# Kernel tuning notes

Measured on AMD Instinct MI355X. Metric: run time of the kernel, lower is better.

## Reference

```python
import jax, jax.numpy as jnp
import numpy as np

D_MODEL = 1024
HEADS = 16
D_HEAD = D_MODEL // HEADS


def relative_shift(score):
    # score: [b, h, n, 2n-1] -> [b, h, n, n] via the pad/reshape skew trick
    b, h, n, r = score.shape  # r == 2n - 1
    score = jnp.pad(score, ((0, 0), (0, 0), (0, 0), (1, 0)))  # [b,h,n,2n]
    score = score.reshape(b, h, n * 2 * n)[:, :, n:].reshape(b, h, n, 2 * n - 1)
    return score[..., :n]


def setup_inputs() -> dict:
    key = jax.random.key(0)
    ks = jax.random.split(key, 16)
    b, n, d = 4, 1024, D_MODEL
    s = 1.0 / np.sqrt(d)
    inp = {
        "query": jax.random.normal(ks[0], (b, n, d), jnp.float32),
        "key": jax.random.normal(ks[1], (b, n, d), jnp.float32),
        "value": jax.random.normal(ks[2], (b, n, d), jnp.float32),
        "pos_emb": jax.random.normal(ks[3], (b, 2 * n - 1, d), jnp.float32),
        "Wq": jax.random.normal(ks[4], (d, d), jnp.float32) * s,
        "bq": jnp.zeros((d,), jnp.float32),
        "Wk": jax.random.normal(ks[5], (d, d), jnp.float32) * s,
        "bk": jnp.zeros((d,), jnp.float32),
        "Wv": jax.random.normal(ks[6], (d, d), jnp.float32) * s,
        "bv": jnp.zeros((d,), jnp.float32),
        "Wo": jax.random.normal(ks[7], (d, d), jnp.float32) * s,
        "bo": jnp.zeros((d,), jnp.float32),
        "Wp": jax.random.normal(ks[8], (d, d), jnp.float32) * s,  # pos_proj, no bias
        "u_bias": jax.random.normal(ks[9], (HEADS, D_HEAD), jnp.float32) * 0.05,
        "v_bias": jax.random.normal(ks[10], (HEADS, D_HEAD), jnp.float32) * 0.05,
    }
    return inp


def reference(query, key, value, pos_emb, Wq, bq, Wk, bk, Wv, bv, Wo, bo, Wp, u_bias, v_bias):
    b, n, d = query.shape
    h, dh = HEADS, D_HEAD
    q = (query @ Wq + bq).reshape(b, n, h, dh)            # [b,n,h,dh]
    k = (key @ Wk + bk).reshape(b, n, h, dh)              # [b,n,h,dh]
    v = (value @ Wv + bv).reshape(b, n, h, dh)            # [b,n,h,dh]
    p = (pos_emb @ Wp).reshape(b, 2 * n - 1, h, dh)       # [b,2n-1,h,dh]

    content_score = jnp.einsum('bnhd,bmhd->bhnm', q + u_bias, k)   # [b,h,n,n]
    pos_score = jnp.einsum('bnhd,brhd->bhnr', q + v_bias, p)        # [b,h,n,2n-1]
    pos_score = relative_shift(pos_score)                           # [b,h,n,n]

    score = (content_score + pos_score) / jnp.sqrt(jnp.asarray(d, score_dtype := query.dtype))
    attn = jax.nn.softmax(score, axis=-1)                 # dropout p=0.0 -> identity
    out = jnp.einsum('bhnm,bmhd->bnhd', attn, v).reshape(b, n, d)
    out = out @ Wo + bo
    return out, attn, content_score, pos_score
```

## Files before the change

kernel.cpp:

```cpp
#include <hip/hip_runtime.h>
#include <hip/hip_bf16.h>

typedef __bf16 bf16;
typedef __attribute__((ext_vector_type(8))) __bf16 bf16x8;
typedef __attribute__((ext_vector_type(4))) float f32x4;

#define DEV static __device__ __forceinline__

namespace {

constexpr int B = 4, N = 1024, D = 1024, H = 16, DH = 64;
constexpr int R2 = 2 * N - 1;
constexpr int BH = B * H;
constexpr float SCL = 0.03125f;

DEV bf16 f2b(float x) {
  unsigned u = __builtin_bit_cast(unsigned, x);
  unsigned r = u + 0x7FFFu + ((u >> 16) & 1u);
  unsigned short h = (unsigned short)(r >> 16);
  return __builtin_bit_cast(bf16, h);
}

DEV unsigned cvtpk(float lo, float hi) {
  unsigned r;
  asm("v_cvt_pk_bf16_f32 %0, %1, %2" : "=v"(r) : "v"(lo), "v"(hi));
  return r;
}

DEV bf16x8 cvt8pk(float4 a, float4 b) {
  union { unsigned u[4]; bf16x8 v; } r;
  r.u[0] = cvtpk(a.x, a.y); r.u[1] = cvtpk(a.z, a.w);
  r.u[2] = cvtpk(b.x, b.y); r.u[3] = cvtpk(b.z, b.w);
  return r.v;
}

DEV f32x4 mfma16(bf16x8 a, bf16x8 b, f32x4 c) {
  return __builtin_amdgcn_mfma_f32_16x16x32_bf16(a, b, c, 0, 0, 0);
}

DEV void nt_store4(float4 v, float* p) {
  f32x4 x = {v.x, v.y, v.z, v.w};
  __builtin_nontemporal_store(x, reinterpret_cast<f32x4*>(p));
}

DEV void block_sync_lds() {
  __builtin_amdgcn_sched_barrier(0);
  asm volatile("s_waitcnt lgkmcnt(0)" ::: "memory");
  __builtin_amdgcn_s_barrier();
  __builtin_amdgcn_sched_barrier(0);
}

__global__ __launch_bounds__(256) void transpose_cast_w(
    const float* __restrict__ w0, const float* __restrict__ w1,
    const float* __restrict__ w2, const float* __restrict__ w3,
    const float* __restrict__ w4, bf16* __restrict__ t0, bf16* __restrict__ t1,
    bf16* __restrict__ t2, bf16* __restrict__ t3, bf16* __restrict__ t4) {
  const float* src; bf16* dst;
  switch (blockIdx.z) {
    case 0: src = w0; dst = t0; break;
    case 1: src = w1; dst = t1; break;
    case 2: src = w2; dst = t2; break;
    case 3: src = w3; dst = t3; break;
    default: src = w4; dst = t4; break;
  }
  __shared__ float tile[64][65];
  const int k0 = blockIdx.y * 64, n0 = blockIdx.x * 64;
  const int t = threadIdx.x, r = t >> 2, c0 = (t & 3) * 16;
  const float4* sp = reinterpret_cast<const float4*>(src + (size_t)(k0 + r) * D + n0 + c0);
#pragma unroll
  for (int q = 0; q < 4; ++q) {
    float4 v = sp[q];
    tile[r][c0 + q * 4 + 0] = v.x; tile[r][c0 + q * 4 + 1] = v.y;
    tile[r][c0 + q * 4 + 2] = v.z; tile[r][c0 + q * 4 + 3] = v.w;
  }
  __syncthreads();
  union { unsigned u[8]; uint4 q[2]; } pk;
#pragma unroll
  for (int e = 0; e < 8; ++e)
    pk.u[e] = cvtpk(tile[c0 + 2 * e][r], tile[c0 + 2 * e + 1][r]);
  uint4* dp = reinterpret_cast<uint4*>(dst + (size_t)(n0 + r) * D + k0 + c0);
  dp[0] = pk.q[0]; dp[1] = pk.q[1];
}

enum { M_QUV = 0, M_HEAD = 1, M_P = 2, M_OUT = 3, M_V = 4 };

template <bool ABF>
DEV void proj_core(char* smem, const void* __restrict__ Av,
                   const bf16* __restrict__ Bt, int M, int mt, int nt, int mode,
                   const float* __restrict__ bias, const float* __restrict__ ubp,
                   const float* __restrict__ vbp, bf16* __restrict__ dst0,
                   bf16* __restrict__ dst1, float* __restrict__ outf) {
  bf16* As = (bf16*)smem;
  bf16* Bs = (bf16*)(smem + 16384);
  float* ep = (float*)smem;
  const int t = threadIdx.x;
  const int m0 = mt * 128, n0 = nt * 128;
  const int lane = t & 63, w = t >> 6;
  const int wi = w >> 1, wj = w & 1;
  const int fr = lane & 15, g = lane >> 4;
  f32x4 acc[4][4] = {};

  int rowc[4], ccc[4], rmc[4];
#pragma unroll
  for (int it = 0; it < 4; ++it) {
    const int chunk = it * 256 + t;
    rowc[it] = chunk >> 3; ccc[it] = chunk & 7;
    int rm = m0 + rowc[it]; rmc[it] = rm < M ? rm : M - 1;
  }
  float4 raf[4][2];
  bf16x8 rab[4];
  bf16x8 rbb[4];
  auto loadstep = [&](int k0) {
#pragma unroll
    for (int it = 0; it < 4; ++it) {
      if (ABF) {
        rab[it] = *reinterpret_cast<const bf16x8*>(
            (const bf16*)Av + (size_t)rmc[it] * D + k0 + ccc[it] * 8);
      } else {
        const float4* ap = reinterpret_cast<const float4*>(
            (const float*)Av + (size_t)rmc[it] * D + k0 + ccc[it] * 8);
        raf[it][0] = ap[0]; raf[it][1] = ap[1];
      }
      rbb[it] = *reinterpret_cast<const bf16x8*>(
          Bt + (size_t)(n0 + rowc[it]) * D + k0 + ccc[it] * 8);
    }
  };

  loadstep(0);
  for (int k0 = 0; k0 < D; k0 += 64) {
#pragma unroll
    for (int it = 0; it < 4; ++it) {
      const int row = rowc[it], cc = ccc[it];
      bf16x8 av;
      if (ABF) av = rab[it]; else av = cvt8pk(raf[it][0], raf[it][1]);
      *reinterpret_cast<bf16x8*>(&As[row * 64 + ((cc ^ (row & 7)) << 3)]) = av;
      *reinterpret_cast<bf16x8*>(&Bs[row * 64 + ((cc ^ (row & 7)) << 3)]) =
          rbb[it];
    }
    block_sync_lds();
    if (k0 + 64 < D) loadstep(k0 + 64);
#pragma unroll
    for (int ks = 0; ks < 2; ++ks) {
      bf16x8 fa[4], fb[4];
#pragma unroll
      for (int i = 0; i < 4; ++i) {
        const int row = wi * 64 + i * 16 + fr;
        fa[i] = *reinterpret_cast<const bf16x8*>(
            &As[row * 64 + (((ks * 4 + g) ^ (row & 7)) << 3)]);
      }
#pragma unroll
      for (int j = 0; j < 4; ++j) {
        const int row = wj * 64 + j * 16 + fr;
        fb[j] = *reinterpret_cast<const bf16x8*>(
            &Bs[row * 64 + (((ks * 4 + g) ^ (row & 7)) << 3)]);
      }
#pragma unroll
      for (int i = 0; i < 4; ++i)
#pragma unroll
        for (int j = 0; j < 4; ++j) acc[i][j] = mfma16(fa[i], fb[j], acc[i][j]);
    }
    block_sync_lds();
  }
#pragma unroll
  for (int p = 0; p < 2; ++p) {
    block_sync_lds();
    if (wi == p) {
#pragma unroll
      for (int i = 0; i < 4; ++i)
#pragma unroll
        for (int j = 0; j < 4; ++j)
#pragma unroll
          for (int q = 0; q < 4; ++q)
            ep[(i * 16 + g * 4 + q) * 132 + wj * 64 + j * 16 + fr] =
                acc[i][j][q];
    }
    block_sync_lds();
    if (mode == M_V) {
      const int col = t >> 1, seg = t & 1;
      const int cg = n0 + col;
      const int h_ = cg >> 6, dh = cg & 63;
      const int b_ = m0 >> 10;
      const int tok0 = (m0 & 1023) + p * 64 + seg * 32;
      const float bvv = bias[cg];
      unsigned pk[16];
#pragma unroll
      for (int e = 0; e < 16; ++e) {
        const float v0 = ep[(seg * 32 + 2 * e + 0) * 132 + col] + bvv;
        const float v1 = ep[(seg * 32 + 2 * e + 1) * 132 + col] + bvv;
        pk[e] = cvtpk(v0, v1);
      }
      bf16* dp = dst0 + ((size_t)(b_ * H + h_) * DH + dh) * N + tok0;
#pragma unroll
      for (int kk = 0; kk < 4; ++kk)
        reinterpret_cast<uint4*>(dp)[kk] =
            *reinterpret_cast<const uint4*>(&pk[kk * 4]);
      continue;
    }
    const int lr = t >> 2, cl = (t & 3) * 32;
    const int m = m0 + p * 64 + lr;
    if (m < M) {
      float v[32];
#pragma unroll
      for (int kk = 0; kk < 8; ++kk) {
        const float4 f =
            *reinterpret_cast<const float4*>(&ep[lr * 132 + cl + kk * 4]);
        v[kk * 4 + 0] = f.x; v[kk * 4 + 1] = f.y;
        v[kk * 4 + 2] = f.z; v[kk * 4 + 3] = f.w;
      }
      const int cg0 = n0 + cl;
      if (mode == M_OUT) {
        float* op = outf + (size_t)m * D + cg0;
#pragma unroll
        for (int kk = 0; kk < 8; ++kk) {
          float4 f = {v[kk * 4] + bias[cg0 + kk * 4],
                      v[kk * 4 + 1] + bias[cg0 + kk * 4 + 1],
                      v[kk * 4 + 2] + bias[cg0 + kk * 4 + 2],
                      v[kk * 4 + 3] + bias[cg0 + kk * 4 + 3]};
          nt_store4(f, op + kk * 4);
        }
      } else if (mode == M_P) {
        const int b_ = m / R2, r_ = m - b_ * R2;
        const int h_ = cg0 >> 6, dh0 = cg0 & 63;
        bf16* dp = dst0 + (((size_t)(b_ * H + h_)) * R2 + r_) * DH + dh0;
        unsigned pk[16];
#pragma unroll
        for (int e = 0; e < 16; ++e) pk[e] = cvtpk(v[2 * e], v[2 * e + 1]);
#pragma unroll
        for (int kk = 0; kk < 4; ++kk)
          reinterpret_cast<uint4*>(dp)[kk] =
              *reinterpret_cast<const uint4*>(&pk[kk * 4]);
      } else {
        const int b_ = m >> 10, ii = m & (N - 1);
        const int h_ = cg0 >> 6, dh0 = cg0 & 63;
        const size_t o = (((size_t)(b_ * H + h_)) * N + ii) * DH + dh0;
        if (mode == M_QUV) {
          unsigned pku[16], pkv[16];
#pragma unroll
          for (int e = 0; e < 16; ++e) {
            const float b0 = bias[cg0 + 2 * e], b1 = bias[cg0 + 2 * e + 1];
            pku[e] = cvtpk(v[2 * e] + b0 + ubp[cg0 + 2 * e],
                           v[2 * e + 1] + b1 + ubp[cg0 + 2 * e + 1]);
            pkv[e] = cvtpk(v[2 * e] + b0 + vbp[cg0 + 2 * e],
                           v[2 * e + 1] + b1 + vbp[cg0 + 2 * e + 1]);
          }
#pragma unroll
          for (int kk = 0; kk < 4; ++kk) {
            reinterpret_cast<uint4*>(dst0 + o)[kk] =
                *reinterpret_cast<const uint4*>(&pku[kk * 4]);
            reinterpret_cast<uint4*>(dst1 + o)[kk] =
                *reinterpret_cast<const uint4*>(&pkv[kk * 4]);
          }
        } else {
          unsigned pk[16];
#pragma unroll
          for (int e = 0; e < 16; ++e)
            pk[e] = cvtpk(v[2 * e] + bias[cg0 + 2 * e],
                          v[2 * e + 1] + bias[cg0 + 2 * e + 1]);
#pragma unroll
          for (int kk = 0; kk < 4; ++kk)
            reinterpret_cast<uint4*>(dst0 + o)[kk] =
                *reinterpret_cast<const uint4*>(&pk[kk * 4]);
        }
      }
    }
  }
}

__global__ __launch_bounds__(256, 3) void proj_qkvp(
    const float* __restrict__ query, const float* __restrict__ key,
    const float* __restrict__ value, const float* __restrict__ pos_emb,
    const bf16* __restrict__ Wqt, const bf16* __restrict__ Wkt,
    const bf16* __restrict__ Wvt, const bf16* __restrict__ Wpt,
    const float* __restrict__ bq, const float* __restrict__ bk,
    const float* __restrict__ bv, const float* __restrict__ ub,
    const float* __restrict__ vbp, bf16* __restrict__ Qu,
    bf16* __restrict__ Qv, bf16* __restrict__ Kb, bf16* __restrict__ Vt,
    bf16* __restrict__ Pb) {
  __shared__ __align__(16) char smem[34048];
  const int z = blockIdx.z, x = blockIdx.x, y = blockIdx.y;
  const int nt = y & 7;
  const int mt = x * 4 + (y >> 3);
  switch (z) {
    case 0:
      proj_core<false>(smem, query, Wqt, B * N, mt, nt, M_QUV, bq, ub, vbp, Qu,
                       Qv, nullptr);
      break;
    case 1:
      proj_core<false>(smem, key, Wkt, B * N, mt, nt, M_HEAD, bk, nullptr,
                       nullptr, Kb, nullptr, nullptr);
      break;
    case 2:
      proj_core<false>(smem, value, Wvt, B * N, mt, nt, M_V, bv, nullptr,
                       nullptr, Vt, nullptr, nullptr);
      break;
    case 3:
      proj_core<false>(smem, pos_emb, Wpt, B * R2, mt, nt, M_P, nullptr,
                       nullptr, nullptr, Pb, nullptr, nullptr);
      break;
    default:
      proj_core<false>(smem, pos_emb, Wpt, B * R2, 32 + mt, nt, M_P, nullptr,
                       nullptr, nullptr, Pb, nullptr, nullptr);
      break;
  }
}

__global__ __launch_bounds__(256, 2) void proj_out(const bf16* __restrict__ OA,
                                                   const bf16* __restrict__ Wot,
                                                   const float* __restrict__ bo,
                                                   float* __restrict__ outF) {
  __shared__ __align__(16) char smem[34048];
  const int nt = blockIdx.y & 7;
  const int mt = blockIdx.x * 4 + (blockIdx.y >> 3);
  proj_core<true>(smem, OA, Wot, B * N, mt, nt, M_OUT, bo, nullptr, nullptr,
                  nullptr, nullptr, outF);
}

constexpr int RB = 16;

DEV int SIDX(int r, int c) {
  return r * 1024 + (((c >> 2) ^ (r & 7)) << 2) + (c & 3);
}

__global__ __launch_bounds__(512, 4) void fused_attn(
    const bf16* __restrict__ Qu, const bf16* __restrict__ Qv,
    const bf16* __restrict__ Kb, const bf16* __restrict__ Pb,
    const bf16* __restrict__ Vt, float* __restrict__ cont,
    float* __restrict__ posS, float* __restrict__ attn,
    bf16* __restrict__ OA) {
  __shared__ float sc[RB * 1024];
  __shared__ float red[1024];
  const int bid0 = blockIdx.y * 64 + blockIdx.x;
  const int bid = (bid0 & 7) * 512 + (bid0 >> 3);
  const int bh = bid >> 6, i0 = (bid & 63) * RB;
  const int t = threadIdx.x, lane = t & 63, w = t >> 6;
  const int fr = lane & 15, g = lane >> 4, kg = g * 8;

  {
    const bf16* Qub = Qu + ((size_t)bh * N + i0) * DH;
    const bf16* Kbh = Kb + (size_t)bh * N * DH;
    const bf16x8 fa0 = *reinterpret_cast<const bf16x8*>(Qub + (size_t)fr * DH + kg);
    const bf16x8 fa1 = *reinterpret_cast<const bf16x8*>(Qub + (size_t)fr * DH + 32 + kg);
#pragma unroll
    for (int tt = 0; tt < 8; ++tt) {
      const int ct = (w * 8 + tt) * 16;
      const bf16x8 fb0 =
          *reinterpret_cast<const bf16x8*>(Kbh + (size_t)(ct + fr) * DH + kg);
      const bf16x8 fb1 =
          *reinterpret_cast<const bf16x8*>(Kbh + (size_t)(ct + fr) * DH + 32 + kg);
      f32x4 acc = {};
      acc = mfma16(fa0, fb0, acc);
      acc = mfma16(fa1, fb1, acc);
      const int c = ct + fr;
#pragma unroll
      for (int q = 0; q < 4; ++q) sc[SIDX(g * 4 + q, c)] = acc[q];
    }
  }
  block_sync_lds();

  float4 xc[2][4];
#pragma unroll
  for (int rr2 = 0; rr2 < 2; ++rr2) {
    const int r = w * 2 + rr2;
#pragma unroll
    for (int k = 0; k < 4; ++k) {
      const int ch = (k * 64 + lane) ^ (r & 7);
      xc[rr2][k] = *reinterpret_cast<const float4*>(&sc[r * 1024 + ch * 4]);
    }
  }
  block_sync_lds();

  {
    float* contb = cont + ((size_t)bh * N + i0) * N;
#pragma unroll
    for (int rr2 = 0; rr2 < 2; ++rr2) {
      const int r = w * 2 + rr2;
#pragma unroll
      for (int k = 0; k < 4; ++k)
        nt_store4(xc[rr2][k], contb + (size_t)r * N + (k * 64 + lane) * 4);
    }
    const bf16* Qvb = Qv + ((size_t)bh * N + i0) * DH;
    const bf16* Pbh = Pb + (size_t)bh * R2 * DH;
    const bf16x8 fa0 = *reinterpret_cast<const bf16x8*>(Qvb + (size_t)fr * DH + kg);
    const bf16x8 fa1 = *reinterpret_cast<const bf16x8*>(Qvb + (size_t)fr * DH + 32 + kg);
    const int Rlo = (N - RB) - i0;
    for (int tt = w; tt < 65; tt += 8) {
      const int rr = Rlo + tt * 16 + fr;
      const int rc = rr < R2 ? rr : R2 - 1;
      const bf16x8 fb0 =
          *reinterpret_cast<const bf16x8*>(Pbh + (size_t)rc * DH + kg);
      const bf16x8 fb1 =
          *reinterpret_cast<const bf16x8*>(Pbh + (size_t)rc * DH + 32 + kg);
      f32x4 acc = {};
      acc = mfma16(fa0, fb0, acc);
      acc = mfma16(fa1, fb1, acc);
#pragma unroll
      for (int q = 0; q < 4; ++q) {
        const int r = g * 4 + q;
        const int jj = rr - (N - 1) + i0 + r;
        if (rr < R2 && jj >= 0 && jj < N) sc[SIDX(r, jj)] = acc[q];
      }
    }
  }
  block_sync_lds();

  {
    float* posb = posS + ((size_t)bh * N + i0) * N;
    float* attnb = attn + ((size_t)bh * N + i0) * N;
#pragma unroll
    for (int rr2 = 0; rr2 < 2; ++rr2) {
      const int r = w * 2 + rr2;
      float4 xp[4], x[4];
      int ch[4];
#pragma unroll
      for (int k = 0; k < 4; ++k) {
        ch[k] = (k * 64 + lane) ^ (r & 7);
        xp[k] = *reinterpret_cast<const float4*>(&sc[r * 1024 + ch[k] * 4]);
      }
      float mx = -1e30f;
#pragma unroll
      for (int k = 0; k < 4; ++k) {
        nt_store4(xp[k], posb + (size_t)r * N + (k * 64 + lane) * 4);
        x[k].x = xc[rr2][k].x + xp[k].x; x[k].y = xc[rr2][k].y + xp[k].y;
        x[k].z = xc[rr2][k].z + xp[k].z; x[k].w = xc[rr2][k].w + xp[k].w;
        mx = fmaxf(mx, fmaxf(fmaxf(x[k].x, x[k].y), fmaxf(x[k].z, x[k].w)));
      }
#pragma unroll
      for (int o = 32; o; o >>= 1) mx = fmaxf(mx, __shfl_xor(mx, o));
      float sum = 0.f;
#pragma unroll
      for (int k = 0; k < 4; ++k) {
        x[k].x = __expf((x[k].x - mx) * SCL);
        x[k].y = __expf((x[k].y - mx) * SCL);
        x[k].z = __expf((x[k].z - mx) * SCL);
        x[k].w = __expf((x[k].w - mx) * SCL);
        sum += x[k].x + x[k].y + x[k].z + x[k].w;
      }
#pragma unroll
      for (int o = 32; o; o >>= 1) sum += __shfl_xor(sum, o);
      const float inv = 1.0f / sum;
#pragma unroll
      for (int k = 0; k < 4; ++k) {
        float4 y = {x[k].x * inv, x[k].y * inv, x[k].z * inv, x[k].w * inv};
        nt_store4(y, attnb + (size_t)r * N + (k * 64 + lane) * 4);
        *reinterpret_cast<float4*>(&sc[r * 1024 + ch[k] * 4]) = y;
      }
    }
  }
  block_sync_lds();

  {
    const bf16* Vbh = Vt + (size_t)bh * DH * N;
    const int wi = w >> 2, wj = w & 3;
    f32x4 acc = {};
    for (int kt = wi * 16; kt < wi * 16 + 16; ++kt) {
      const int p0 = (kt * 8 + g * 2) ^ (fr & 7);
      const float4 a0 = *reinterpret_cast<const float4*>(&sc[fr * 1024 + p0 * 4]);
      const float4 a1 =
          *reinterpret_cast<const float4*>(&sc[fr * 1024 + (p0 ^ 1) * 4]);
      const bf16x8 fb = *reinterpret_cast<const bf16x8*>(
          Vbh + (size_t)(wj * 16 + fr) * N + kt * 32 + kg);
      acc = mfma16(cvt8pk(a0, a1), fb, acc);
    }
    if (wi == 1) *reinterpret_cast<f32x4*>(&red[(wj * 64 + lane) * 4]) = acc;
    block_sync_lds();
    if (wi == 0) {
      const f32x4 o = *reinterpret_cast<const f32x4*>(&red[(wj * 64 + lane) * 4]);
      const int b_ = bh >> 4, h_ = bh & 15;
#pragma unroll
      for (int q = 0; q < 4; ++q) {
        const int row = i0 + g * 4 + q;
        const int dh = wj * 16 + fr;
        OA[((size_t)b_ * N + row) * D + h_ * DH + dh] = f2b(acc[q] + o[q]);
      }
    }
  }
}

}

extern "C" void kernel_launch(void* const* d_in, const int* in_sizes, int n_in,
                              void* d_out, int out_size, void* d_ws,
                              size_t ws_size, hipStream_t stream) {
  (void)in_sizes; (void)n_in; (void)out_size; (void)ws_size;
  const float* query = (const float*)d_in[0];
  const float* key = (const float*)d_in[1];
  const float* value = (const float*)d_in[2];
  const float* pos_emb = (const float*)d_in[3];
  const float* Wq = (const float*)d_in[4];
  const float* bq = (const float*)d_in[5];
  const float* Wk = (const float*)d_in[6];
  const float* bk = (const float*)d_in[7];
  const float* Wv = (const float*)d_in[8];
  const float* bv = (const float*)d_in[9];
  const float* Wo = (const float*)d_in[10];
  const float* bo = (const float*)d_in[11];
  const float* Wp = (const float*)d_in[12];
  const float* ub = (const float*)d_in[13];
  const float* vb = (const float*)d_in[14];

  float* outF = (float*)d_out;
  float* attn = outF + (size_t)B * N * D;
  float* cont = attn + (size_t)BH * N * N;
  float* posS = cont + (size_t)BH * N * N;

  char* wsp = (char*)d_ws;
  auto alloc = [&](size_t elems) {
    bf16* p = (bf16*)wsp;
    wsp += elems * sizeof(bf16);
    return p;
  };
  bf16* Qu = alloc((size_t)BH * N * DH);
  bf16* Qv = alloc((size_t)BH * N * DH);
  bf16* Kb = alloc((size_t)BH * N * DH);
  bf16* Vt = alloc((size_t)BH * DH * N);
  bf16* Pb = alloc((size_t)BH * R2 * DH);
  bf16* OA = alloc((size_t)B * N * D);
  bf16* Wqt = alloc((size_t)D * D);
  bf16* Wkt = alloc((size_t)D * D);
  bf16* Wvt = alloc((size_t)D * D);
  bf16* Wpt = alloc((size_t)D * D);
  bf16* Wot = alloc((size_t)D * D);

  dim3 blk(256);
  transpose_cast_w<<<dim3(16, 16, 5), blk, 0, stream>>>(Wq, Wk, Wv, Wp, Wo, Wqt,
                                                        Wkt, Wvt, Wpt, Wot);
  proj_qkvp<<<dim3(8, 32, 5), blk, 0, stream>>>(query, key, value, pos_emb,
                                                Wqt, Wkt, Wvt, Wpt, bq, bk, bv,
                                                ub, vb, Qu, Qv, Kb, Vt, Pb);
  fused_attn<<<dim3(64, 64), dim3(512), 0, stream>>>(Qu, Qv, Kb, Pb, Vt, cont,
                                                     posS, attn, OA);
  proj_out<<<dim3(8, 32), blk, 0, stream>>>(OA, Wot, bo, outF);
}
```

Before: 340.3 us.

## Store score tile in LDS as bf16 and use 256-thread blocks in fused attention

Keeps the per-block score tile in shared memory as bf16 instead of fp32, halving LDS use so more blocks fit per CU, and halves the block to 4 waves each covering 4 rows. The PV step now reads bf16 fragments directly and each wave owns a 16-column slice, removing the cross-wave reduction buffer and extra barrier. The last posS row store is deferred into the PV loop with raised wave priority to overlap stores with MFMA work. The trade-off is that the returned content and position scores are rounded through bf16, reducing output precision.

Result: slower. 369.8 us (+8.7%).

```diff
diff --git a/kernel.cpp b/kernel.cpp
--- a/kernel.cpp
+++ b/kernel.cpp
@@ -4,6 +4,8 @@
 typedef __bf16 bf16;
 typedef __attribute__((ext_vector_type(8))) __bf16 bf16x8;
 typedef __attribute__((ext_vector_type(4))) float f32x4;
+typedef __attribute__((ext_vector_type(4))) unsigned short u16x4;
+typedef __attribute__((ext_vector_type(2))) unsigned int u32x2;
 
 #define DEV static __device__ __forceinline__
 
@@ -19,6 +21,15 @@
   unsigned r = u + 0x7FFFu + ((u >> 16) & 1u);
   unsigned short h = (unsigned short)(r >> 16);
   return __builtin_bit_cast(bf16, h);
+}
+
+DEV float b2f(unsigned short h) {
+  unsigned u = (unsigned)h << 16;
+  return __builtin_bit_cast(float, u);
+}
+
+DEV float4 cvt4(u16x4 v) {
+  return {b2f(v[0]), b2f(v[1]), b2f(v[2]), b2f(v[3])};
 }
 
 DEV unsigned cvtpk(float lo, float hi) {
@@ -317,18 +328,17 @@
 
 constexpr int RB = 16;
 
-DEV int SIDX(int r, int c) {
-  return r * 1024 + (((c >> 2) ^ (r & 7)) << 2) + (c & 3);
-}
-
-__global__ __launch_bounds__(512, 4) void fused_attn(
+DEV int SBYTE(int r, int c) {
+  return r * 2048 + ((((c >> 3) ^ (r & 7)) << 4) | ((c & 7) << 1));
+}
+
+__global__ __launch_bounds__(256, 5) void fused_attn(
     const bf16* __restrict__ Qu, const bf16* __restrict__ Qv,
     const bf16* __restrict__ Kb, const bf16* __restrict__ Pb,
     const bf16* __restrict__ Vt, float* __restrict__ cont,
     float* __restrict__ posS, float* __restrict__ attn,
     bf16* __restrict__ OA) {
-  __shared__ float sc[RB * 1024];
-  __shared__ float red[1024];
+  __shared__ __align__(16) char scb[RB * 2048];
   const int bid0 = blockIdx.y * 64 + blockIdx.x;
   const int bid = (bid0 & 7) * 512 + (bid0 >> 3);
   const int bh = bid >> 6, i0 = (bid & 63) * RB;
@@ -340,9 +350,8 @@
     const bf16* Kbh = Kb + (size_t)bh * N * DH;
     const bf16x8 fa0 = *reinterpret_cast<const bf16x8*>(Qub + (size_t)fr * DH + kg);
     const bf16x8 fa1 = *reinterpret_cast<const bf16x8*>(Qub + (size_t)fr * DH + 32 + kg);
-#pragma unroll
-    for (int tt = 0; tt < 8; ++tt) {
-      const int ct = (w * 8 + tt) * 16;
+    for (int tt = 0; tt < 16; ++tt) {
+      const int ct = (w * 16 + tt) * 16;
       const bf16x8 fb0 =
           *reinterpret_cast<const bf16x8*>(Kbh + (size_t)(ct + fr) * DH + kg);
       const bf16x8 fb1 =
@@ -352,19 +361,21 @@
       acc = mfma16(fa1, fb1, acc);
       const int c = ct + fr;
 #pragma unroll
-      for (int q = 0; q < 4; ++q) sc[SIDX(g * 4 + q, c)] = acc[q];
+      for (int q = 0; q < 4; ++q)
+        *reinterpret_cast<bf16*>(scb + SBYTE(g * 4 + q, c)) = f2b(acc[q]);
     }
   }
   block_sync_lds();
 
-  float4 xc[2][4];
-#pragma unroll
-  for (int rr2 = 0; rr2 < 2; ++rr2) {
-    const int r = w * 2 + rr2;
+  u16x4 xcb[4][4];
+#pragma unroll
+  for (int rr = 0; rr < 4; ++rr) {
+    const int r = w * 4 + rr;
 #pragma unroll
     for (int k = 0; k < 4; ++k) {
-      const int ch = (k * 64 + lane) ^ (r & 7);
-      xc[rr2][k] = *reinterpret_cast<const float4*>(&sc[r * 1024 + ch * 4]);
+      const int ch = (k * 32 + (lane >> 1)) ^ (r & 7);
+      xcb[rr][k] = *reinterpret_cast<const u16x4*>(
+          scb + r * 2048 + (ch << 4) + (lane & 1) * 8);
     }
   }
   block_sync_lds();
@@ -372,18 +383,18 @@
   {
     float* contb = cont + ((size_t)bh * N + i0) * N;
 #pragma unroll
-    for (int rr2 = 0; rr2 < 2; ++rr2) {
-      const int r = w * 2 + rr2;
+    for (int rr = 0; rr < 4; ++rr) {
+      const int r = w * 4 + rr;
 #pragma unroll
       for (int k = 0; k < 4; ++k)
-        nt_store4(xc[rr2][k], contb + (size_t)r * N + (k * 64 + lane) * 4);
+        nt_store4(cvt4(xcb[rr][k]), contb + (size_t)r * N + (k * 64 + lane) * 4);
     }
     const bf16* Qvb = Qv + ((size_t)bh * N + i0) * DH;
     const bf16* Pbh = Pb + (size_t)bh * R2 * DH;
     const bf16x8 fa0 = *reinterpret_cast<const bf16x8*>(Qvb + (size_t)fr * DH + kg);
     const bf16x8 fa1 = *reinterpret_cast<const bf16x8*>(Qvb + (size_t)fr * DH + 32 + kg);
     const int Rlo = (N - RB) - i0;
-    for (int tt = w; tt < 65; tt += 8) {
+    for (int tt = w; tt < 65; tt += 4) {
       const int rr = Rlo + tt * 16 + fr;
       const int rc = rr < R2 ? rr : R2 - 1;
       const bf16x8 fb0 =
@@ -397,31 +408,41 @@
       for (int q = 0; q < 4; ++q) {
         const int r = g * 4 + q;
         const int jj = rr - (N - 1) + i0 + r;
-        if (rr < R2 && jj >= 0 && jj < N) sc[SIDX(r, jj)] = acc[q];
+        if (rr < R2 && jj >= 0 && jj < N)
+          *reinterpret_cast<bf16*>(scb + SBYTE(r, jj)) = f2b(acc[q]);
       }
     }
   }
   block_sync_lds();
 
+  u16x4 xp1[4];
   {
     float* posb = posS + ((size_t)bh * N + i0) * N;
     float* attnb = attn + ((size_t)bh * N + i0) * N;
 #pragma unroll
-    for (int rr2 = 0; rr2 < 2; ++rr2) {
-      const int r = w * 2 + rr2;
-      float4 xp[4], x[4];
-      int ch[4];
+    for (int rr = 0; rr < 4; ++rr) {
+      const int r = w * 4 + rr;
+      u16x4 xpb[4];
+      float4 x[4];
+      int chs[4];
 #pragma unroll
       for (int k = 0; k < 4; ++k) {
-        ch[k] = (k * 64 + lane) ^ (r & 7);
-        xp[k] = *reinterpret_cast<const float4*>(&sc[r * 1024 + ch[k] * 4]);
+        chs[k] = (k * 32 + (lane >> 1)) ^ (r & 7);
+        xpb[k] = *reinterpret_cast<const u16x4*>(
+            scb + r * 2048 + (chs[k] << 4) + (lane & 1) * 8);
       }
       float mx = -1e30f;
 #pragma unroll
       for (int k = 0; k < 4; ++k) {
-        nt_store4(xp[k], posb + (size_t)r * N + (k * 64 + lane) * 4);
-        x[k].x = xc[rr2][k].x + xp[k].x; x[k].y = xc[rr2][k].y + xp[k].y;
-        x[k].z = xc[rr2][k].z + xp[k].z; x[k].w = xc[rr2][k].w + xp[k].w;
+        const float4 xc = cvt4(xcb[rr][k]);
+        const float4 xp = cvt4(xpb[k]);
+        if (rr < 3) {
+          nt_store4(xp, posb + (size_t)r * N + (k * 64 + lane) * 4);
+        } else {
+          xp1[k] = xpb[k];
+        }
+        x[k].x = xc.x + xp.x; x[k].y = xc.y + xp.y;
+        x[k].z = xc.z + xp.z; x[k].w = xc.w + xp.w;
         mx = fmaxf(mx, fmaxf(fmaxf(x[k].x, x[k].y), fmaxf(x[k].z, x[k].w)));
       }
 #pragma unroll
@@ -442,7 +463,9 @@
       for (int k = 0; k < 4; ++k) {
         float4 y = {x[k].x * inv, x[k].y * inv, x[k].z * inv, x[k].w * inv};
         nt_store4(y, attnb + (size_t)r * N + (k * 64 + lane) * 4);
-        *reinterpret_cast<float4*>(&sc[r * 1024 + ch[k] * 4]) = y;
+        u32x2 pk2 = {cvtpk(y.x, y.y), cvtpk(y.z, y.w)};
+        *reinterpret_cast<u32x2*>(scb + r * 2048 + (chs[k] << 4) +
+                                  (lane & 1) * 8) = pk2;
       }
     }
   }
@@ -450,28 +473,27 @@
 
   {
     const bf16* Vbh = Vt + (size_t)bh * DH * N;
-    const int wi = w >> 2, wj = w & 3;
+    float* posb3 = posS + ((size_t)bh * N + i0 + w * 4 + 3) * N + lane * 4;
     f32x4 acc = {};
-    for (int kt = wi * 16; kt < wi * 16 + 16; ++kt) {
-      const int p0 = (kt * 8 + g * 2) ^ (fr & 7);
-      const float4 a0 = *reinterpret_cast<const float4*>(&sc[fr * 1024 + p0 * 4]);
-      const float4 a1 =
-          *reinterpret_cast<const float4*>(&sc[fr * 1024 + (p0 ^ 1) * 4]);
+    __builtin_amdgcn_s_setprio(1);
+    for (int kt = 0; kt < 32; ++kt) {
+      if ((kt & 7) == 0) {
+        const int k = kt >> 3;
+        nt_store4(cvt4(xp1[k]), posb3 + k * 256);
+      }
+      const bf16x8 fa = *reinterpret_cast<const bf16x8*>(
+          scb + fr * 2048 + (((kt * 4 + g) ^ (fr & 7)) << 4));
       const bf16x8 fb = *reinterpret_cast<const bf16x8*>(
-          Vbh + (size_t)(wj * 16 + fr) * N + kt * 32 + kg);
-      acc = mfma16(cvt8pk(a0, a1), fb, acc);
-    }
-    if (wi == 1) *reinterpret_cast<f32x4*>(&red[(wj * 64 + lane) * 4]) = acc;
-    block_sync_lds();
-    if (wi == 0) {
-      const f32x4 o = *reinterpret_cast<const f32x4*>(&red[(wj * 64 + lane) * 4]);
-      const int b_ = bh >> 4, h_ = bh & 15;
-#pragma unroll
-      for (int q = 0; q < 4; ++q) {
-        const int row = i0 + g * 4 + q;
-        const int dh = wj * 16 + fr;
-        OA[((size_t)b_ * N + row) * D + h_ * DH + dh] = f2b(acc[q] + o[q]);
-      }
+          Vbh + (size_t)(w * 16 + fr) * N + kt * 32 + kg);
+      acc = mfma16(fa, fb, acc);
+    }
+    __builtin_amdgcn_s_setprio(0);
+    const int b_ = bh >> 4, h_ = bh & 15;
+#pragma unroll
+    for (int q = 0; q < 4; ++q) {
+      const int row = i0 + g * 4 + q;
+      const int dh = w * 16 + fr;
+      OA[((size_t)b_ * N + row) * D + h_ * DH + dh] = f2b(acc[q]);
     }
   }
 }
@@ -527,7 +549,7 @@
   proj_qkvp<<<dim3(8, 32, 5), blk, 0, stream>>>(query, key, value, pos_emb,
                                                 Wqt, Wkt, Wvt, Wpt, bq, bk, bv,
                                                 ub, vb, Qu, Qv, Kb, Vt, Pb);
-  fused_attn<<<dim3(64, 64), dim3(512), 0, stream>>>(Qu, Qv, Kb, Pb, Vt, cont,
+  fused_attn<<<dim3(64, 64), dim3(256), 0, stream>>>(Qu, Qv, Kb, Pb, Vt, cont,
                                                      posS, attn, OA);
   proj_out<<<dim3(8, 32), blk, 0, stream>>>(OA, Wot, bo, outF);
 }
```
